# Performance work log

Measured on AMD Instinct MI355X. Metric: run time of the kernel, lower is better.

Reference implementation:

```python
import jax, jax.numpy as jnp
import numpy as np

B, S, D, H = 4, 1024, 1024, 16
DK = D // H  # 64; concat head dim is 2*DK


def setup_inputs() -> dict:
    key = jax.random.key(0)
    ks = jax.random.split(key, 32)
    inp = {}
    for i, name in enumerate(["query_g", "key_g", "query_a", "key_a", "value_a"]):
        inp[name] = jax.random.normal(ks[i], (B, S, D), dtype=jnp.float32)
    inp["mask"] = jnp.ones((B, S, S), dtype=jnp.int32)
    w_scale = 1.0 / np.sqrt(D).astype(np.float32)
    # torch Linear weights are [out, in]; y = x @ W.T + b
    param_shapes = [
        ("Wqg", (D, D)), ("bqg", (D,)), ("Wkg", (D, D)), ("bkg", (D,)),
        ("Wqa", (D, D)), ("bqa", (D,)), ("Wka", (D, D)), ("bka", (D,)),
        ("Wva", (D, D)), ("bva", (D,)),
        ("Wgate", (D, 2 * D)), ("bgate", (D,)),
        ("Winfo", (D, D)), ("binfo", (D,)),
    ]
    for j, (name, shape) in enumerate(param_shapes):
        inp[name] = jax.random.normal(ks[5 + j], shape, dtype=jnp.float32) * w_scale
    return inp


def reference(query_g, key_g, query_a, key_a, value_a, mask,
              Wqg, bqg, Wkg, bkg, Wqa, bqa, Wka, bka, Wva, bva,
              Wgate, bgate, Winfo, binfo):
    def heads(x, W, b):
        # [B,S,D] -> [B,H,S,DK]
        return (x @ W.T + b).reshape(B, S, H, DK).transpose(0, 2, 1, 3)

    qg = heads(query_g, Wqg, bqg)
    kg = heads(key_g, Wkg, bkg)
    qa = heads(query_a, Wqa, bqa)
    ka = heads(key_a, Wka, bka)
    va = heads(value_a, Wva, bva)

    q = jnp.concatenate([qa, qg], axis=-1)  # [B,H,S,2*DK]
    k = jnp.concatenate([ka, kg], axis=-1)
    scores = jnp.einsum('bhqd,bhkd->bhqk', q, k) / np.float32(np.sqrt(2 * DK))
    scores = jnp.where(mask[:, None, :, :] == 0, jnp.float32(-1e9), scores)
    p_attn = jax.nn.softmax(scores, axis=-1)  # dropout is identity in eval
    x = jnp.einsum('bhqk,bhkd->bhqd', p_attn, va)
    x = x.transpose(0, 2, 1, 3).reshape(B, S, D)

    # GLU branch (dropout_glu is identity in eval); linears_out is identity
    gate = jax.nn.sigmoid(jnp.concatenate([query_a, query_g], axis=-1) @ Wgate.T + bgate)
    info = x @ Winfo.T + binfo
    return gate * info
```

## Files before the change

kernel.cpp:

```cpp
#include <hip/hip_runtime.h>


typedef unsigned short u16;
typedef __bf16 bf16x8 __attribute__((ext_vector_type(8)));
typedef float f32x4 __attribute__((ext_vector_type(4)));

#define DEV static __device__ __forceinline__

DEV u16 f2bf(float x) {
  union { __bf16 h; u16 u; } c;
  c.h = (__bf16)x;
  return c.u;
}
DEV float bf2f(u16 h) { return __uint_as_float(((unsigned)h) << 16); }

DEV bf16x8 cvt8(float4 a, float4 b) {
  bf16x8 v;
  v[0] = (__bf16)a.x; v[1] = (__bf16)a.y; v[2] = (__bf16)a.z; v[3] = (__bf16)a.w;
  v[4] = (__bf16)b.x; v[5] = (__bf16)b.y; v[6] = (__bf16)b.z; v[7] = (__bf16)b.w;
  return v;
}

DEV void gload_lds16(const void* g, void* l) {
  __builtin_amdgcn_global_load_lds(
      (const __attribute__((address_space(1))) void*)g,
      (__attribute__((address_space(3))) void*)l, 16, 0, 0);
}

struct CvtArgs {
  const float* src[12];
  u16* dst[12];
  int n8[12];
};

__global__ __launch_bounds__(256) void cvt_kernel(CvtArgs C) {
  const int stride = gridDim.x * blockDim.x;
#pragma unroll 1
  for (int s = 0; s < 12; ++s) {
    const float4* src = (const float4*)C.src[s];
    u16* dst = C.dst[s];
    const int n8 = C.n8[s];
    for (int i = blockIdx.x * blockDim.x + threadIdx.x; i < n8; i += stride) {
      const float4 a = src[i * 2];
      const float4 b = src[i * 2 + 1];
      *(bf16x8*)(void*)(dst + (size_t)i * 8) = cvt8(a, b);
    }
  }
}

struct ArgsD {
  const u16* act[5];
  const u16* W[7];
  const float* bias[7];
  u16 *q_buf, *k_buf, *va_t, *x_buf, *g_buf;
  float* out;
};

__global__ __launch_bounds__(256, 4) void gemm_dma(ArgsD P, int unit_override) {
  __shared__ __align__(16) u16 As[2][128 * 32];
  __shared__ __align__(16) u16 Bs[2][128 * 32];

  int unit, bid;
  if (unit_override >= 0) { unit = unit_override; bid = blockIdx.x; }
  else { unit = blockIdx.x >> 8; bid = blockIdx.x & 255; }
  const int bm = bid & 31;
  const int bn = bid >> 5;

  const int tid = threadIdx.x;
  const int lane = tid & 63;
  const int wid = tid >> 6;
  const int wq = wid >> 1, wn = wid & 1;
  const int cl = lane & 15;
  const int gl = lane >> 4;

  const u16 *A0, *A1 = nullptr, *Wp;
  const float* bp;
  int nkt, mode;
  switch (unit) {
    case 0: A0 = P.act[0]; A1 = P.act[1]; Wp = P.W[5]; bp = P.bias[5]; nkt = 64; mode = 0; break;
    case 1: A0 = P.act[0]; Wp = P.W[0]; bp = P.bias[0]; nkt = 32; mode = 1; break;
    case 2: A0 = P.act[1]; Wp = P.W[1]; bp = P.bias[1]; nkt = 32; mode = 2; break;
    case 3: A0 = P.act[2]; Wp = P.W[2]; bp = P.bias[2]; nkt = 32; mode = 3; break;
    case 4: A0 = P.act[3]; Wp = P.W[3]; bp = P.bias[3]; nkt = 32; mode = 4; break;
    case 5: A0 = P.act[4]; Wp = P.W[4]; bp = P.bias[4]; nkt = 32; mode = 5; break;
    default: A0 = P.x_buf; Wp = P.W[6]; bp = P.bias[6]; nkt = 32; mode = 6; break;
  }
  const int K = nkt * 32;

  f32x4 acc[4][4];
  const f32x4 vzero = {0.f, 0.f, 0.f, 0.f};
#pragma unroll
  for (int i = 0; i < 4; i++)
#pragma unroll
    for (int j = 0; j < 4; j++) acc[i][j] = vzero;

  int drow[2];
  const int dcol = (lane & 3) * 8;
  drow[0] = (wid * 2 + 0) * 16 + (lane >> 2);
  drow[1] = (wid * 2 + 1) * 16 + (lane >> 2);

  auto STAGE = [&](int kt, int buf) {
    const u16* Ab;
    int akoff;
    if (A1 && kt >= 32) { Ab = A1; akoff = (kt - 32) * 32; }
    else { Ab = A0; akoff = kt * 32; }
#pragma unroll
    for (int i = 0; i < 2; ++i) {
      gload_lds16(Ab + (size_t)(bm * 128 + drow[i]) * 1024 + akoff + dcol,
                  &As[buf][(wid * 2 + i) * 512]);
      gload_lds16(Wp + (size_t)(bn * 128 + drow[i]) * K + kt * 32 + dcol,
                  &Bs[buf][(wid * 2 + i) * 512]);
    }
  };

  STAGE(0, 0);

  for (int kt = 0; kt < nkt; ++kt) {
    const int cur = kt & 1;
    __builtin_amdgcn_sched_barrier(0);
    __builtin_amdgcn_s_barrier();
    if (kt + 1 < nkt) {
      STAGE(kt + 1, cur ^ 1);
      asm volatile("s_waitcnt vmcnt(4)" ::: "memory");
    } else {
      asm volatile("s_waitcnt vmcnt(0)" ::: "memory");
    }
    __builtin_amdgcn_s_barrier();
    __builtin_amdgcn_sched_barrier(0);

    bf16x8 af[4], bfr[4];
#pragma unroll
    for (int mi = 0; mi < 4; mi++)
      af[mi] = *(const bf16x8*)(const void*)&As[cur][(wq * 64 + mi * 16 + cl) * 32 + gl * 8];
#pragma unroll
    for (int nj = 0; nj < 4; nj++)
      bfr[nj] = *(const bf16x8*)(const void*)&Bs[cur][(wn * 64 + nj * 16 + cl) * 32 + gl * 8];

#pragma unroll
    for (int mi = 0; mi < 4; mi++)
#pragma unroll
      for (int nj = 0; nj < 4; nj++)
        acc[mi][nj] = __builtin_amdgcn_mfma_f32_16x16x32_bf16(af[mi], bfr[nj], acc[mi][nj], 0, 0, 0);
  }

  const int rowbase = bm * 128 + wq * 64;
  const int colbase = bn * 128 + wn * 64;
#pragma unroll
  for (int mi = 0; mi < 4; mi++) {
#pragma unroll
    for (int nj = 0; nj < 4; nj++) {
      const int gn = colbase + nj * 16 + cl;
      const float bias = bp[gn];
      const int gm0 = rowbase + mi * 16 + gl * 4;
      if (mode == 0) {
#pragma unroll
        for (int r = 0; r < 4; r++) {
          float v = acc[mi][nj][r] + bias;
          float s = 1.0f / (1.0f + __expf(-v));
          size_t idx = (size_t)(gm0 + r) * 1024 + gn;
          if (P.g_buf) P.g_buf[idx] = f2bf(s);
          else P.out[idx] = s;
        }
      } else if (mode <= 4) {
        u16* dst = (mode <= 2) ? P.q_buf : P.k_buf;
        const int part = (mode == 2 || mode == 4) ? 1 : 0;
        const int h = gn >> 6, dk = gn & 63;
#pragma unroll
        for (int r = 0; r < 4; r++) {
          int gm = gm0 + r;
          int b = gm >> 10, s = gm & 1023;
          dst[(((size_t)(b * 16 + h)) * 1024 + s) * 128 + part * 64 + dk] =
              f2bf(acc[mi][nj][r] + bias);
        }
      } else if (mode == 5) {
        const int h = gn >> 6, dk = gn & 63;
        int b = gm0 >> 10, s = gm0 & 1023;
        ushort4 pk;
        pk.x = f2bf(acc[mi][nj][0] + bias);
        pk.y = f2bf(acc[mi][nj][1] + bias);
        pk.z = f2bf(acc[mi][nj][2] + bias);
        pk.w = f2bf(acc[mi][nj][3] + bias);
        *(ushort4*)&P.va_t[(((size_t)(b * 16 + h)) * 64 + dk) * 1024 + s] = pk;
      } else {
#pragma unroll
        for (int r = 0; r < 4; r++) {
          size_t idx = (size_t)(gm0 + r) * 1024 + gn;
          float g = P.g_buf ? bf2f(P.g_buf[idx]) : P.out[idx];
          P.out[idx] = (acc[mi][nj][r] + bias) * g;
        }
      }
    }
  }
}

struct Args {
  const float* act[5];
  const float* W[7];
  const float* bias[7];
  u16 *q_buf, *k_buf, *va_t, *x_buf, *g_buf;
  float* out;
};

__global__ __launch_bounds__(256, 2) void gemm_kernel(Args P, int unit_override) {
  __shared__ __align__(16) u16 As[128 * 40];
  __shared__ __align__(16) u16 Bs[128 * 40];

  int unit, bid;
  if (unit_override >= 0) { unit = unit_override; bid = blockIdx.x; }
  else { unit = blockIdx.x >> 8; bid = blockIdx.x & 255; }
  const int bm = bid & 31;
  const int bn = bid >> 5;

  const int tid = threadIdx.x;
  const int lane = tid & 63;
  const int wid = tid >> 6;
  const int wq = wid >> 1, wn = wid & 1;
  const int cl = lane & 15;
  const int gl = lane >> 4;

  const float *A0, *A1 = nullptr, *Wp, *bp;
  int nkt, mode;
  switch (unit) {
    case 0: A0 = P.act[0]; A1 = P.act[1]; Wp = P.W[5]; bp = P.bias[5]; nkt = 64; mode = 0; break;
    case 1: A0 = P.act[0]; Wp = P.W[0]; bp = P.bias[0]; nkt = 32; mode = 1; break;
    case 2: A0 = P.act[1]; Wp = P.W[1]; bp = P.bias[1]; nkt = 32; mode = 2; break;
    case 3: A0 = P.act[2]; Wp = P.W[2]; bp = P.bias[2]; nkt = 32; mode = 3; break;
    case 4: A0 = P.act[3]; Wp = P.W[3]; bp = P.bias[3]; nkt = 32; mode = 4; break;
    case 5: A0 = P.act[4]; Wp = P.W[4]; bp = P.bias[4]; nkt = 32; mode = 5; break;
    default: A0 = nullptr; Wp = P.W[6]; bp = P.bias[6]; nkt = 32; mode = 6; break;
  }
  const int K = nkt * 32;

  f32x4 acc[4][4];
  const f32x4 vzero = {0.f, 0.f, 0.f, 0.f};
#pragma unroll
  for (int i = 0; i < 4; i++)
#pragma unroll
    for (int j = 0; j < 4; j++) acc[i][j] = vzero;

  int arow[2], apn[2];
#pragma unroll
  for (int j = 0; j < 2; j++) {
    int f = (wid * 2 + j) * 64 + lane;
    arow[j] = f >> 2;
    apn[j] = f & 3;
  }

  float4 ra[2][2], rb[2][2];
  bf16x8 ra6[2];

  auto stage = [&](int kt) {
    const float* Abase;
    int akoff;
    if (A1 && kt >= 32) { Abase = A1; akoff = (kt - 32) * 32; }
    else { Abase = A0; akoff = kt * 32; }
#pragma unroll
    for (int j = 0; j < 2; j++) {
      size_t ae = (size_t)(bm * 128 + arow[j]) * 1024 + akoff + apn[j] * 8;
      size_t we = (size_t)(bn * 128 + arow[j]) * K + kt * 32 + apn[j] * 8;
      if (mode == 6) {
        ra6[j] = *(const bf16x8*)(const void*)(P.x_buf + ae);
      } else {
        const float* p = Abase + ae;
        ra[j][0] = *(const float4*)(const void*)p;
        ra[j][1] = *(const float4*)(const void*)(p + 4);
      }
      const float* q = Wp + we;
      rb[j][0] = *(const float4*)(const void*)q;
      rb[j][1] = *(const float4*)(const void*)(q + 4);
    }
  };

  stage(0);

  for (int kt = 0; kt < nkt; kt++) {
    __syncthreads();
#pragma unroll
    for (int j = 0; j < 2; j++) {
      *(bf16x8*)(void*)&As[arow[j] * 40 + apn[j] * 8] =
          (mode == 6) ? ra6[j] : cvt8(ra[j][0], ra[j][1]);
      *(bf16x8*)(void*)&Bs[arow[j] * 40 + apn[j] * 8] = cvt8(rb[j][0], rb[j][1]);
    }
    __syncthreads();

    bf16x8 af[4], bfr[4];
#pragma unroll
    for (int mi = 0; mi < 4; mi++)
      af[mi] = *(const bf16x8*)(const void*)&As[(wq * 64 + mi * 16 + cl) * 40 + gl * 8];
#pragma unroll
    for (int nj = 0; nj < 4; nj++)
      bfr[nj] = *(const bf16x8*)(const void*)&Bs[(wn * 64 + nj * 16 + cl) * 40 + gl * 8];

    if (kt + 1 < nkt) stage(kt + 1);

#pragma unroll
    for (int mi = 0; mi < 4; mi++)
#pragma unroll
      for (int nj = 0; nj < 4; nj++)
        acc[mi][nj] = __builtin_amdgcn_mfma_f32_16x16x32_bf16(af[mi], bfr[nj], acc[mi][nj], 0, 0, 0);
  }

  const int rowbase = bm * 128 + wq * 64;
  const int colbase = bn * 128 + wn * 64;
#pragma unroll
  for (int mi = 0; mi < 4; mi++) {
#pragma unroll
    for (int nj = 0; nj < 4; nj++) {
      const int gn = colbase + nj * 16 + cl;
      const float bias = bp[gn];
      const int gm0 = rowbase + mi * 16 + gl * 4;
      if (mode == 0) {
#pragma unroll
        for (int r = 0; r < 4; r++) {
          float v = acc[mi][nj][r] + bias;
          float s = 1.0f / (1.0f + __expf(-v));
          size_t idx = (size_t)(gm0 + r) * 1024 + gn;
          if (P.g_buf) P.g_buf[idx] = f2bf(s);
          else P.out[idx] = s;
        }
      } else if (mode <= 4) {
        u16* dst = (mode <= 2) ? P.q_buf : P.k_buf;
        const int part = (mode == 2 || mode == 4) ? 1 : 0;
        const int h = gn >> 6, dk = gn & 63;
#pragma unroll
        for (int r = 0; r < 4; r++) {
          int gm = gm0 + r;
          int b = gm >> 10, s = gm & 1023;
          dst[(((size_t)(b * 16 + h)) * 1024 + s) * 128 + part * 64 + dk] =
              f2bf(acc[mi][nj][r] + bias);
        }
      } else if (mode == 5) {
        const int h = gn >> 6, dk = gn & 63;
        int b = gm0 >> 10, s = gm0 & 1023;
        ushort4 pk;
        pk.x = f2bf(acc[mi][nj][0] + bias);
        pk.y = f2bf(acc[mi][nj][1] + bias);
        pk.z = f2bf(acc[mi][nj][2] + bias);
        pk.w = f2bf(acc[mi][nj][3] + bias);
        *(ushort4*)&P.va_t[(((size_t)(b * 16 + h)) * 64 + dk) * 1024 + s] = pk;
      } else {
#pragma unroll
        for (int r = 0; r < 4; r++) {
          size_t idx = (size_t)(gm0 + r) * 1024 + gn;
          float g = P.g_buf ? bf2f(P.g_buf[idx]) : P.out[idx];
          P.out[idx] = (acc[mi][nj][r] + bias) * g;
        }
      }
    }
  }
}

__global__ __launch_bounds__(256, 2) void attn_kernel(const u16* __restrict__ q_buf,
                                                      const u16* __restrict__ k_buf,
                                                      const u16* __restrict__ va_t,
                                                      const int* __restrict__ mask,
                                                      u16* __restrict__ x_buf) {
  __shared__ __align__(16) u16 Ks[64 * 136];
  __shared__ __align__(16) u16 Vs[64 * 72];
  __shared__ __align__(16) u16 Ps[4 * 32 * 72];
  __shared__ int mflags[16];

  const int tid = threadIdx.x;
  const int lane = tid & 63;
  const int wid = tid >> 6;
  const int cl = lane & 15;
  const int gl = lane >> 4;

  const int qt = blockIdx.x & 7;
  const int bh = blockIdx.x >> 3;
  const int b = bh >> 4, h = bh & 15;
  const u16* qh = q_buf + (size_t)bh * 1024 * 128;
  const u16* kh = k_buf + (size_t)bh * 1024 * 128;
  const u16* vh = va_t + (size_t)bh * 64 * 1024;
  const int s0 = qt * 128;

  if (tid < 16) mflags[tid] = 1;
  __syncthreads();
  {
    const int* mbase = mask + ((size_t)b * 1024 + s0) * 1024 + tid * 4;
    int ok = 1;
#pragma unroll 4
    for (int i = 0; i < 128; i++) {
      const int4 m4 = *(const int4*)(const void*)(mbase + (size_t)i * 1024);
      if (!(m4.x && m4.y && m4.z && m4.w)) ok = 0;
    }
    if (!ok) atomicAnd(&mflags[tid >> 4], 0);
  }
  __syncthreads();

  bf16x8 aq[2][4];
#pragma unroll
  for (int mi = 0; mi < 2; mi++) {
    int row = s0 + wid * 32 + mi * 16 + cl;
#pragma unroll
    for (int kk = 0; kk < 4; kk++)
      aq[mi][kk] = *(const bf16x8*)(const void*)&qh[(size_t)row * 128 + kk * 32 + gl * 8];
  }

  f32x4 acc_o[2][4];
  float l_part[2][4];
  const f32x4 vzero = {0.f, 0.f, 0.f, 0.f};
#pragma unroll
  for (int mi = 0; mi < 2; mi++) {
#pragma unroll
    for (int nj = 0; nj < 4; nj++) acc_o[mi][nj] = vzero;
#pragma unroll
    for (int r = 0; r < 4; r++) l_part[mi][r] = 0.f;
  }

  const float scale = 0.08838834764831845f;
  u16* pw = &Ps[wid * 32 * 72];

  int krow[4], kp[4], vrow[2], vp[2];
#pragma unroll
  for (int j = 0; j < 4; j++) {
    int f = (wid * 4 + j) * 64 + lane;
    krow[j] = f >> 4; kp[j] = f & 15;
  }
#pragma unroll
  for (int j = 0; j < 2; j++) {
    int f = (wid * 2 + j) * 64 + lane;
    vrow[j] = f >> 3; vp[j] = f & 7;
  }

  bf16x8 kv[4], vv[2];
  auto stageKV = [&](int kt) {
#pragma unroll
    for (int j = 0; j < 4; j++)
      kv[j] = *(const bf16x8*)(const void*)&kh[(size_t)(kt * 64 + krow[j]) * 128 + kp[j] * 8];
#pragma unroll
    for (int j = 0; j < 2; j++)
      vv[j] = *(const bf16x8*)(const void*)&vh[(size_t)vrow[j] * 1024 + kt * 64 + vp[j] * 8];
  };

  stageKV(0);

  for (int kt = 0; kt < 16; kt++) {
    __syncthreads();
#pragma unroll
    for (int j = 0; j < 4; j++)
      *(bf16x8*)(void*)&Ks[krow[j] * 136 + kp[j] * 8] = kv[j];
#pragma unroll
    for (int j = 0; j < 2; j++)
      *(bf16x8*)(void*)&Vs[vrow[j] * 72 + vp[j] * 8] = vv[j];
    __syncthreads();

    if (kt < 15) stageKV(kt + 1);

    f32x4 sc[2][4];
#pragma unroll
    for (int mi = 0; mi < 2; mi++)
#pragma unroll
      for (int nj = 0; nj < 4; nj++) sc[mi][nj] = vzero;
#pragma unroll
    for (int kk = 0; kk < 4; kk++) {
      bf16x8 bk[4];
#pragma unroll
      for (int nj = 0; nj < 4; nj++)
        bk[nj] = *(const bf16x8*)(const void*)&Ks[(nj * 16 + cl) * 136 + (kk * 4 + gl) * 8];
#pragma unroll
      for (int mi = 0; mi < 2; mi++)
#pragma unroll
        for (int nj = 0; nj < 4; nj++)
          sc[mi][nj] = __builtin_amdgcn_mfma_f32_16x16x32_bf16(aq[mi][kk], bk[nj], sc[mi][nj], 0, 0, 0);
    }

    const bool fastm = (mflags[kt] != 0);
#pragma unroll
    for (int mi = 0; mi < 2; mi++) {
#pragma unroll
      for (int nj = 0; nj < 4; nj++) {
        int key = kt * 64 + nj * 16 + cl;
#pragma unroll
        for (int r = 0; r < 4; r++) {
          int lrow = mi * 16 + gl * 4 + r;
          float sv = fminf(sc[mi][nj][r] * scale, 30.0f);
          float pv;
          if (fastm) {
            pv = __expf(sv);
          } else {
            int qrow = s0 + wid * 32 + lrow;
            int mv = mask[((size_t)b * 1024 + qrow) * 1024 + key];
            pv = (mv != 0) ? __expf(sv) : 0.0f;
          }
          l_part[mi][r] += pv;
          pw[lrow * 72 + nj * 16 + cl] = f2bf(pv);
        }
      }
    }

#pragma unroll
    for (int kk = 0; kk < 2; kk++) {
      bf16x8 ap[2], bv[4];
#pragma unroll
      for (int mi = 0; mi < 2; mi++)
        ap[mi] = *(const bf16x8*)(const void*)&pw[(mi * 16 + cl) * 72 + kk * 32 + gl * 8];
#pragma unroll
      for (int nj = 0; nj < 4; nj++)
        bv[nj] = *(const bf16x8*)(const void*)&Vs[(nj * 16 + cl) * 72 + (kk * 4 + gl) * 8];
#pragma unroll
      for (int mi = 0; mi < 2; mi++)
#pragma unroll
        for (int nj = 0; nj < 4; nj++)
          acc_o[mi][nj] = __builtin_amdgcn_mfma_f32_16x16x32_bf16(ap[mi], bv[nj], acc_o[mi][nj], 0, 0, 0);
    }
  }

#pragma unroll
  for (int mi = 0; mi < 2; mi++)
#pragma unroll
    for (int r = 0; r < 4; r++) {
      float s = l_part[mi][r];
      s += __shfl_xor(s, 1);
      s += __shfl_xor(s, 2);
      s += __shfl_xor(s, 4);
      s += __shfl_xor(s, 8);
      l_part[mi][r] = 1.0f / s;
    }

#pragma unroll
  for (int mi = 0; mi < 2; mi++)
#pragma unroll
    for (int nj = 0; nj < 4; nj++)
#pragma unroll
      for (int r = 0; r < 4; r++) {
        int srow = s0 + wid * 32 + mi * 16 + gl * 4 + r;
        int dv = nj * 16 + cl;
        float v = acc_o[mi][nj][r] * l_part[mi][r];
        x_buf[((size_t)b * 1024 + srow) * 1024 + h * 64 + dv] = f2bf(v);
      }
}

extern "C" void kernel_launch(void* const* d_in, const int* in_sizes, int n_in,
                              void* d_out, int out_size, void* d_ws, size_t ws_size,
                              hipStream_t stream) {
  (void)in_sizes; (void)n_in; (void)out_size;
  const int* mask = (const int*)d_in[5];

  char* ws = (char*)d_ws;
  u16* q_buf = (u16*)(ws);
  u16* k_buf = (u16*)(ws + ((size_t)16 << 20));
  u16* va_t  = (u16*)(ws + ((size_t)32 << 20));
  u16* x_buf = (u16*)(ws + ((size_t)40 << 20));
  u16* g_buf = (ws_size >= ((size_t)56 << 20)) ? (u16*)(ws + ((size_t)48 << 20)) : nullptr;

  const int act_idx[5] = {2, 0, 3, 1, 4};
  const int w_idx[7] = {10, 6, 12, 8, 14, 16, 18};
  const int b_idx[7] = {11, 7, 13, 9, 15, 17, 19};

  const bool big = (ws_size >= ((size_t)112 << 20)) && (g_buf != nullptr);

  if (big) {
    u16* actb[5];
    for (int i = 0; i < 5; i++) actb[i] = (u16*)(ws + ((size_t)56 << 20) + (size_t)i * (8 << 20));
    u16* wb[7];
    for (int i = 0; i < 5; i++) wb[i] = (u16*)(ws + ((size_t)96 << 20) + (size_t)i * (2 << 20));
    wb[5] = (u16*)(ws + ((size_t)106 << 20));
    wb[6] = (u16*)(ws + ((size_t)110 << 20));

    CvtArgs C;
    for (int i = 0; i < 5; i++) {
      C.src[i] = (const float*)d_in[act_idx[i]];
      C.dst[i] = actb[i];
      C.n8[i] = (4096 * 1024) / 8;
    }
    for (int i = 0; i < 7; i++) {
      C.src[5 + i] = (const float*)d_in[w_idx[i]];
      C.dst[5 + i] = wb[i];
      C.n8[5 + i] = ((i == 5) ? (1024 * 2048) : (1024 * 1024)) / 8;
    }
    hipLaunchKernelGGL(cvt_kernel, dim3(2048), dim3(256), 0, stream, C);

    ArgsD P;
    for (int i = 0; i < 5; i++) P.act[i] = actb[i];
    for (int i = 0; i < 7; i++) { P.W[i] = wb[i]; P.bias[i] = (const float*)d_in[b_idx[i]]; }
    P.q_buf = q_buf; P.k_buf = k_buf; P.va_t = va_t; P.x_buf = x_buf;
    P.g_buf = g_buf; P.out = (float*)d_out;

    hipLaunchKernelGGL(gemm_dma, dim3(1536), dim3(256), 0, stream, P, -1);
    hipLaunchKernelGGL(attn_kernel, dim3(512), dim3(256), 0, stream,
                       q_buf, k_buf, va_t, mask, x_buf);
    hipLaunchKernelGGL(gemm_dma, dim3(256), dim3(256), 0, stream, P, 6);
  } else {
    Args P;
    for (int i = 0; i < 5; i++) P.act[i] = (const float*)d_in[act_idx[i]];
    for (int i = 0; i < 7; i++) { P.W[i] = (const float*)d_in[w_idx[i]]; P.bias[i] = (const float*)d_in[b_idx[i]]; }
    P.q_buf = q_buf; P.k_buf = k_buf; P.va_t = va_t; P.x_buf = x_buf;
    P.g_buf = g_buf; P.out = (float*)d_out;

    hipLaunchKernelGGL(gemm_kernel, dim3(1536), dim3(256), 0, stream, P, -1);
    hipLaunchKernelGGL(attn_kernel, dim3(512), dim3(256), 0, stream,
                       q_buf, k_buf, va_t, mask, x_buf);
    hipLaunchKernelGGL(gemm_kernel, dim3(256), dim3(256), 0, stream, P, 6);
  }
}
```

Before: 370.2 us.

## Triple-buffer GEMM LDS staging and precompute mask flags in a separate kernel

The bf16 GEMM moves from double to triple buffering of its LDS tiles, keeping two k-tiles in flight. To make room it lowers the launch-bounds occupancy hint from 4 to 3 blocks. Separately, the mask all-ones scan is pulled out of the attention kernel into a dedicated kernel that writes per-tile flags to the workspace. Attention blocks then read those flags instead of each scanning 128 rows of the int32 mask, so the mask is read once rather than redundantly by every head. The costs are an extra kernel launch and possibly lower GEMM occupancy.

```diff
diff --git a/kernel.cpp b/kernel.cpp
--- a/kernel.cpp
+++ b/kernel.cpp
@@ -48,6 +48,29 @@
   }
 }
 
+__global__ __launch_bounds__(256) void maskflags_kernel(const int* __restrict__ mask,
+                                                        int* __restrict__ flags) {
+  const int bid = blockIdx.x;
+  const int kt = bid & 15, qt = (bid >> 4) & 7, b = bid >> 7;
+  const int tid = threadIdx.x;
+  __shared__ int f;
+  if (tid == 0) f = 1;
+  __syncthreads();
+  int ok = 1;
+  const int c = tid & 15;
+  const int r0 = tid >> 4;
+#pragma unroll
+  for (int p = 0; p < 8; ++p) {
+    const int row = qt * 128 + p * 16 + r0;
+    const int4 m4 = *(const int4*)(const void*)(
+        mask + ((size_t)b * 1024 + row) * 1024 + kt * 64 + c * 4);
+    if (!(m4.x && m4.y && m4.z && m4.w)) ok = 0;
+  }
+  if (!ok) atomicAnd(&f, 0);
+  __syncthreads();
+  if (tid == 0) flags[bid] = f;
+}
+
 struct ArgsD {
   const u16* act[5];
   const u16* W[7];
@@ -56,9 +79,9 @@
   float* out;
 };
 
-__global__ __launch_bounds__(256, 4) void gemm_dma(ArgsD P, int unit_override) {
-  __shared__ __align__(16) u16 As[2][128 * 32];
-  __shared__ __align__(16) u16 Bs[2][128 * 32];
+__global__ __launch_bounds__(256, 3) void gemm_dma(ArgsD P, int unit_override) {
+  __shared__ __align__(16) u16 As[3][128 * 32];
+  __shared__ __align__(16) u16 Bs[3][128 * 32];
 
   int unit, bid;
   if (unit_override >= 0) { unit = unit_override; bid = blockIdx.x; }
@@ -114,13 +137,16 @@
   };
 
   STAGE(0, 0);
+  STAGE(1, 1);
 
   for (int kt = 0; kt < nkt; ++kt) {
-    const int cur = kt & 1;
+    const int cur = kt % 3;
     __builtin_amdgcn_sched_barrier(0);
     __builtin_amdgcn_s_barrier();
-    if (kt + 1 < nkt) {
-      STAGE(kt + 1, cur ^ 1);
+    if (kt + 2 < nkt) {
+      STAGE(kt + 2, (kt + 2) % 3);
+      asm volatile("s_waitcnt vmcnt(8)" ::: "memory");
+    } else if (kt + 1 < nkt) {
       asm volatile("s_waitcnt vmcnt(4)" ::: "memory");
     } else {
       asm volatile("s_waitcnt vmcnt(0)" ::: "memory");
@@ -354,6 +380,7 @@
                                                       const u16* __restrict__ k_buf,
                                                       const u16* __restrict__ va_t,
                                                       const int* __restrict__ mask,
+                                                      const int* __restrict__ flags,
                                                       u16* __restrict__ x_buf) {
   __shared__ __align__(16) u16 Ks[64 * 136];
   __shared__ __align__(16) u16 Vs[64 * 72];
@@ -374,9 +401,12 @@
   const u16* vh = va_t + (size_t)bh * 64 * 1024;
   const int s0 = qt * 128;
 
-  if (tid < 16) mflags[tid] = 1;
-  __syncthreads();
-  {
+  if (flags) {
+    if (tid < 16) mflags[tid] = flags[(b * 8 + qt) * 16 + tid];
+    __syncthreads();
+  } else {
+    if (tid < 16) mflags[tid] = 1;
+    __syncthreads();
     const int* mbase = mask + ((size_t)b * 1024 + s0) * 1024 + tid * 4;
     int ok = 1;
 #pragma unroll 4
@@ -385,8 +415,8 @@
       if (!(m4.x && m4.y && m4.z && m4.w)) ok = 0;
     }
     if (!ok) atomicAnd(&mflags[tid >> 4], 0);
-  }
-  __syncthreads();
+    __syncthreads();
+  }
 
   bf16x8 aq[2][4];
 #pragma unroll
@@ -549,6 +579,7 @@
   const int b_idx[7] = {11, 7, 13, 9, 15, 17, 19};
 
   const bool big = (ws_size >= ((size_t)112 << 20)) && (g_buf != nullptr);
+  int* flags = (ws_size >= ((size_t)112 << 20) + 4096) ? (int*)(ws + ((size_t)112 << 20)) : nullptr;
 
   if (big) {
     u16* actb[5];
@@ -569,6 +600,7 @@
       C.dst[5 + i] = wb[i];
       C.n8[5 + i] = ((i == 5) ? (1024 * 2048) : (1024 * 1024)) / 8;
     }
+    if (flags) hipLaunchKernelGGL(maskflags_kernel, dim3(512), dim3(256), 0, stream, mask, flags);
     hipLaunchKernelGGL(cvt_kernel, dim3(2048), dim3(256), 0, stream, C);
 
     ArgsD P;
@@ -579,7 +611,7 @@
 
     hipLaunchKernelGGL(gemm_dma, dim3(1536), dim3(256), 0, stream, P, -1);
     hipLaunchKernelGGL(attn_kernel, dim3(512), dim3(256), 0, stream,
-                       q_buf, k_buf, va_t, mask, x_buf);
+                       q_buf, k_buf, va_t, mask, flags, x_buf);
     hipLaunchKernelGGL(gemm_dma, dim3(256), dim3(256), 0, stream, P, 6);
   } else {
     Args P;
@@ -590,7 +622,7 @@
 
     hipLaunchKernelGGL(gemm_kernel, dim3(1536), dim3(256), 0, stream, P, -1);
     hipLaunchKernelGGL(attn_kernel, dim3(512), dim3(256), 0, stream,
-                       q_buf, k_buf, va_t, mask, x_buf);
+                       q_buf, k_buf, va_t, mask, (const int*)nullptr, x_buf);
     hipLaunchKernelGGL(gemm_kernel, dim3(256), dim3(256), 0, stream, P, 6);
   }
 }
```

After: 354.4 us. 4.3% less time.
